# Kernel optimization log

Measured on AMD Instinct MI355X. Metric: run time of the kernel, lower is better.

Reference implementation:

```python
import jax, jax.numpy as jnp
import numpy as np

N, D, B = 100000, 256, 512


def setup_inputs() -> dict:
    key = jax.random.key(0)
    k1, k2, k3, k4, k5 = jax.random.split(key, 5)
    h_fused = jax.random.normal(k1, (N, D), dtype=jnp.float32)
    V = jax.random.normal(k2, (N, D), dtype=jnp.float32)
    bucket_logits_q = jax.random.normal(k3, (N, B), dtype=jnp.float32)
    bk = jax.random.randint(k4, (N,), 0, B, dtype=jnp.int64)
    W_r = jax.random.normal(k5, (D, D), dtype=jnp.float32) * (1.0 / np.sqrt(D))
    ln_gamma = jnp.ones((D,), dtype=jnp.float32)
    ln_beta = jnp.zeros((D,), dtype=jnp.float32)
    return {"h_fused": h_fused, "V": V, "bucket_logits_q": bucket_logits_q,
            "bk": bk, "W_r": W_r, "ln_gamma": ln_gamma, "ln_beta": ln_beta}


def reference(h_fused, V, bucket_logits_q, bk, W_r, ln_gamma, ln_beta):
    n, d = h_fused.shape
    num_buckets = bucket_logits_q.shape[1]

    p_q = jax.nn.softmax(bucket_logits_q, axis=-1)  # (N, B)

    # Single-pass segment-mean replacing the Python per-bucket loop.
    sums = jax.ops.segment_sum(V, bk, num_segments=num_buckets)          # (B, d)
    counts = jax.ops.segment_sum(jnp.ones((n,), V.dtype), bk,
                                 num_segments=num_buckets)               # (B,)
    prototypes = sums / jnp.maximum(counts, 1.0)[:, None]
    global_mean = V.mean(axis=0)
    prototypes = jnp.where((counts == 0)[:, None], global_mean, prototypes)

    proto_weighted = p_q @ prototypes          # (N, d)
    residual = proto_weighted @ W_r.T          # Linear, no bias

    entropy = -(p_q * jnp.log(p_q + 1e-9)).sum(axis=-1)      # (N,)
    confidence = 1.0 - entropy / jnp.log(jnp.float32(num_buckets))
    gate = (1.0 - confidence)[:, None]

    h = h_fused + gate * residual
    # LayerNorm (eps=1e-5, biased variance, as torch)
    mean = h.mean(axis=-1, keepdims=True)
    var = ((h - mean) ** 2).mean(axis=-1, keepdims=True)
    h_norm = (h - mean) / jnp.sqrt(var + 1e-5) * ln_gamma + ln_beta
    return h_norm, confidence
```

## Files before the change

### kernel.cpp

```cpp
#include <hip/hip_runtime.h>
#include <hip/hip_bf16.h>

#define N_ROWS 100000
#define D 256
#define B 512
#define RT 16
#define RS 260

typedef __attribute__((ext_vector_type(8))) short sh8;
typedef __attribute__((ext_vector_type(4))) float f32x4;

__device__ __forceinline__ float lo16(unsigned u) { return __uint_as_float(u << 16); }
__device__ __forceinline__ float hi16(unsigned u) { return __uint_as_float(u & 0xffff0000u); }
__device__ __forceinline__ unsigned short bf16r(float f) {
    unsigned u = __float_as_uint(f);
    unsigned r = (u + 0x7fffu + ((u >> 16) & 1u)) >> 16;
    return (unsigned short)r;
}

template<bool BH>
__device__ __forceinline__ float ldf(const void* p, size_t i) {
    if constexpr (BH) return lo16(((const unsigned short*)p)[i]);
    else              return ((const float*)p)[i];
}
template<bool BH>
__device__ __forceinline__ void ld8(const void* p, size_t i, float* o) {
    if constexpr (BH) {
        uint4 v = *(const uint4*)((const unsigned short*)p + i);
        o[0]=lo16(v.x); o[1]=hi16(v.x); o[2]=lo16(v.y); o[3]=hi16(v.y);
        o[4]=lo16(v.z); o[5]=hi16(v.z); o[6]=lo16(v.w); o[7]=hi16(v.w);
    } else {
        const float4* q = (const float4*)((const float*)p + i);
        float4 a = q[0], b = q[1];
        o[0]=a.x; o[1]=a.y; o[2]=a.z; o[3]=a.w;
        o[4]=b.x; o[5]=b.y; o[6]=b.z; o[7]=b.w;
    }
}
template<bool BH>
__device__ __forceinline__ void stf(void* p, size_t i, float v) {
    if constexpr (BH) ((unsigned short*)p)[i] = bf16r(v);
    else              ((float*)p)[i] = v;
}

__global__ void sniff_kernel(const unsigned* __restrict__ h, int* __restrict__ flag) {
    if (threadIdx.x == 0 && blockIdx.x == 0) {
        int bad = 0;
        for (int i = 0; i < 128; ++i) {
            unsigned w = h[i];
            unsigned e0 = (w >> 7)  & 0xffu;
            unsigned e1 = (w >> 23) & 0xffu;
            if (e0 > 135u || e1 > 135u) bad = 1;
        }
        *flag = bad ? 0 : 1;
    }
}

template<bool BH>
__device__ __forceinline__ void seg_body(const void* __restrict__ V, const void* __restrict__ bkp,
                                         float* __restrict__ sums, float* __restrict__ counts,
                                         float* __restrict__ gsum) {
    bool is64 = true;
    const long long* b64 = (const long long*)bkp;
    #pragma unroll
    for (int j = 0; j < 16; ++j) {
        long long v = b64[j];
        if (v < 0 || v >= B) is64 = false;
    }
    const int* b32 = (const int*)bkp;
    const int t = threadIdx.x;
    float g = 0.f;
    for (int row = blockIdx.x; row < N_ROWS; row += gridDim.x) {
        int k = is64 ? (int)b64[row] : b32[row];
        float v = ldf<BH>(V, (size_t)row * D + t);
        atomicAdd(&sums[k * D + t], v);
        g += v;
        if (t == 0) atomicAdd(&counts[k], 1.0f);
    }
    atomicAdd(&gsum[t], g);
}
__global__ __launch_bounds__(256) void seg_kernel(const void* V, const void* bk,
                                                  float* sums, float* counts, float* gsum,
                                                  const int* flag) {
    if (*flag) seg_body<true>(V, bk, sums, counts, gsum);
    else       seg_body<false>(V, bk, sums, counts, gsum);
}

template<bool BH>
__device__ __forceinline__ void proto_body(const float* __restrict__ sums,
                                           const float* __restrict__ counts,
                                           const float* __restrict__ gsum,
                                           const void* __restrict__ W_r,
                                           unsigned short* __restrict__ pwB,
                                           float* __restrict__ proto) {
    const int b = blockIdx.x, t = threadIdx.x;
    float c = counts[b];
    proto[t] = (c > 0.5f) ? sums[b * D + t] / c : gsum[t] * (1.0f / N_ROWS);
    __syncthreads();
    float acc = 0.f;
    float w[8];
    #pragma unroll
    for (int c8 = 0; c8 < D / 8; ++c8) {
        ld8<BH>(W_r, (size_t)t * D + c8 * 8, w);
        #pragma unroll
        for (int j = 0; j < 8; ++j) acc = fmaf(proto[c8 * 8 + j], w[j], acc);
    }
    pwB[((size_t)(b >> 3) * 256 + t) * 8 + (b & 7)] = bf16r(acc);
}
__global__ __launch_bounds__(256) void proto_kernel(const float* sums, const float* counts,
                                                    const float* gsum, const void* W_r,
                                                    unsigned short* pwB, const int* flag) {
    __shared__ __align__(16) float proto[D];
    if (*flag) proto_body<true>(sums, counts, gsum, W_r, pwB, proto);
    else       proto_body<false>(sums, counts, gsum, W_r, pwB, proto);
}

template<bool BH>
__device__ __forceinline__ void fused_body(const void* __restrict__ logits,
                                           const void* __restrict__ h_fused,
                                           const unsigned short* __restrict__ pwB,
                                           const void* __restrict__ gamma,
                                           const void* __restrict__ beta,
                                           void* __restrict__ out,
                                           float* __restrict__ smu,
                                           float* __restrict__ part1,
                                           float* __restrict__ part2,
                                           float* __restrict__ gate_lds) {
    const int t = threadIdx.x;
    const long long base_row = (long long)blockIdx.x * RT;

    {
        const int grp = t >> 4, sub = t & 15;
        const long long row = base_row + grp;
        float x[32];
        #pragma unroll
        for (int c = 0; c < 4; ++c)
            ld8<BH>(logits, (size_t)row * B + sub * 32 + c * 8, &x[c * 8]);
        float m = x[0];
        #pragma unroll
        for (int k = 1; k < 32; ++k) m = fmaxf(m, x[k]);
        m = fmaxf(m, __shfl_xor(m, 1));
        m = fmaxf(m, __shfl_xor(m, 2));
        m = fmaxf(m, __shfl_xor(m, 4));
        m = fmaxf(m, __shfl_xor(m, 8));
        float S = 0.f;
        #pragma unroll
        for (int k = 0; k < 32; ++k) { x[k] = __expf(x[k] - m); S += x[k]; }
        S += __shfl_xor(S, 1); S += __shfl_xor(S, 2); S += __shfl_xor(S, 4); S += __shfl_xor(S, 8);
        const float inv = 1.0f / S;
        float ent = 0.f;
        #pragma unroll
        for (int k = 0; k < 32; ++k) {
            float p = x[k] * inv;
            ent = fmaf(p, __logf(p + 1e-9f), ent);
            x[k] = p;
        }
        ent += __shfl_xor(ent, 1); ent += __shfl_xor(ent, 2);
        ent += __shfl_xor(ent, 4); ent += __shfl_xor(ent, 8);
        const float gate = -ent * 0.16035674514745464f;
        unsigned short* A16 = (unsigned short*)smu;
        #pragma unroll
        for (int c = 0; c < 4; ++c) {
            unsigned q0 = (unsigned)bf16r(x[c*8+0]) | ((unsigned)bf16r(x[c*8+1]) << 16);
            unsigned q1 = (unsigned)bf16r(x[c*8+2]) | ((unsigned)bf16r(x[c*8+3]) << 16);
            unsigned q2 = (unsigned)bf16r(x[c*8+4]) | ((unsigned)bf16r(x[c*8+5]) << 16);
            unsigned q3 = (unsigned)bf16r(x[c*8+6]) | ((unsigned)bf16r(x[c*8+7]) << 16);
            *(uint4*)&A16[((size_t)(sub * 4 + c) * 16 + grp) * 8] = make_uint4(q0, q1, q2, q3);
        }
        if (sub == 0) {
            gate_lds[grp] = gate;
            stf<BH>(out, (size_t)N_ROWS * D + row, 1.0f - gate);
        }
    }
    __syncthreads();

    {
        const int l  = t & 63, w = t >> 6;
        const int lr = l & 15, lg = l >> 4;
        f32x4 acc[4];
        const f32x4 fz = {0.f, 0.f, 0.f, 0.f};
        #pragma unroll
        for (int n = 0; n < 4; ++n) acc[n] = fz;
        const uint4* Ap = (const uint4*)smu;
        const uint4* Bp = (const uint4*)pwB;
        #pragma unroll 2
        for (int ks = 0; ks < 16; ++ks) {
            const int kg = ks * 4 + lg;
            sh8 a = __builtin_bit_cast(sh8, Ap[kg * 16 + lr]);
            #pragma unroll
            for (int n = 0; n < 4; ++n) {
                sh8 b = __builtin_bit_cast(sh8, Bp[(size_t)kg * 256 + w * 64 + n * 16 + lr]);
                acc[n] = __builtin_amdgcn_mfma_f32_16x16x32_bf16(a, b, acc[n], 0, 0, 0);
            }
        }
        __syncthreads();
        float* res = smu;
        #pragma unroll
        for (int n = 0; n < 4; ++n)
            #pragma unroll
            for (int r = 0; r < 4; ++r)
                res[(lg * 4 + r) * RS + (w * 64 + n * 16 + lr)] = acc[n][r];
    }
    __syncthreads();

    {
        const float* res = smu;
        const float g  = ldf<BH>(gamma, t);
        const float bt = ldf<BH>(beta, t);
        const int wv = t >> 6, ln = t & 63;
        float hr[RT];
        #pragma unroll
        for (int r = 0; r < RT; ++r) {
            const long long row = base_row + r;
            float hv = fmaf(gate_lds[r], res[r * RS + t], ldf<BH>(h_fused, (size_t)row * D + t));
            hr[r] = hv;
            float s1 = hv, s2 = hv * hv;
            #pragma unroll
            for (int o = 32; o > 0; o >>= 1) { s1 += __shfl_xor(s1, o); s2 += __shfl_xor(s2, o); }
            if (ln == 0) { part1[r * 4 + wv] = s1; part2[r * 4 + wv] = s2; }
        }
        __syncthreads();
        #pragma unroll
        for (int r = 0; r < RT; ++r) {
            float sum = part1[r * 4 + 0] + part1[r * 4 + 1] + part1[r * 4 + 2] + part1[r * 4 + 3];
            float sq  = part2[r * 4 + 0] + part2[r * 4 + 1] + part2[r * 4 + 2] + part2[r * 4 + 3];
            float mean = sum * (1.0f / D);
            float var  = fmaf(-mean, mean, sq * (1.0f / D));
            float rstd = rsqrtf(var + 1e-5f);
            const long long row = base_row + r;
            stf<BH>(out, (size_t)row * D + t, fmaf((hr[r] - mean) * rstd, g, bt));
        }
    }
}
__global__ __launch_bounds__(256, 4) void fused_kernel(const void* logits, const void* h_fused,
                                                       const unsigned short* pwB, const void* gamma,
                                                       const void* beta, void* out, const int* flag) {
    __shared__ __align__(16) float sm[RT * RS + RT * 4 * 2 + RT];
    float* smu      = sm;
    float* part1    = sm + RT * RS;
    float* part2    = part1 + RT * 4;
    float* gate_lds = part2 + RT * 4;
    if (*flag) fused_body<true>(logits, h_fused, pwB, gamma, beta, out,
                                smu, part1, part2, gate_lds);
    else       fused_body<false>(logits, h_fused, pwB, gamma, beta, out,
                                 smu, part1, part2, gate_lds);
}

extern "C" void kernel_launch(void* const* d_in, const int* in_sizes, int n_in,
                              void* d_out, int out_size, void* d_ws, size_t ws_size,
                              hipStream_t stream) {
    const void* h_fused = d_in[0];
    const void* V       = d_in[1];
    const void* logits  = d_in[2];
    const void* bk      = d_in[3];
    const void* W_r     = d_in[4];
    const void* gamma   = d_in[5];
    const void* beta    = d_in[6];

    float* ws      = (float*)d_ws;
    float* sums    = ws;
    float* counts  = ws + 131072;
    float* gsum    = ws + 131584;
    unsigned short* pwB = (unsigned short*)(ws + 131840);
    int*   flag    = (int*)(ws + 131840 + 65536);

    hipMemsetAsync(d_ws, 0, (size_t)131840 * sizeof(float), stream);
    sniff_kernel<<<1, 64, 0, stream>>>((const unsigned*)h_fused, flag);
    seg_kernel<<<1024, 256, 0, stream>>>(V, bk, sums, counts, gsum, flag);
    proto_kernel<<<B, 256, 0, stream>>>(sums, counts, gsum, W_r, pwB, flag);
    fused_kernel<<<N_ROWS / RT, 256, 0, stream>>>(logits, h_fused, pwB, gamma, beta, d_out, flag);
}
```

Baseline: 668.9 us.

## Replace atomic segment-sum with counting-sort and per-bucket gather reduction

```diff
diff --git a/kernel.cpp b/kernel.cpp
--- a/kernel.cpp
+++ b/kernel.cpp
@@ -42,6 +42,17 @@
     else              ((float*)p)[i] = v;
 }
 
+__device__ __forceinline__ bool bk_is64(const void* bkp) {
+    bool is64 = true;
+    const long long* b64 = (const long long*)bkp;
+    #pragma unroll
+    for (int j = 0; j < 16; ++j) {
+        long long v = b64[j];
+        if (v < 0 || v >= B) is64 = false;
+    }
+    return is64;
+}
+
 __global__ void sniff_kernel(const unsigned* __restrict__ h, int* __restrict__ flag) {
     if (threadIdx.x == 0 && blockIdx.x == 0) {
         int bad = 0;
@@ -55,34 +66,94 @@
     }
 }
 
-template<bool BH>
-__device__ __forceinline__ void seg_body(const void* __restrict__ V, const void* __restrict__ bkp,
-                                         float* __restrict__ sums, float* __restrict__ counts,
-                                         float* __restrict__ gsum) {
-    bool is64 = true;
+__global__ __launch_bounds__(256) void hist_kernel(const void* __restrict__ bkp,
+                                                   float* __restrict__ counts) {
+    const bool is64 = bk_is64(bkp);
     const long long* b64 = (const long long*)bkp;
+    const int* b32 = (const int*)bkp;
+    const int stride = gridDim.x * 256;
+    for (int row = blockIdx.x * 256 + threadIdx.x; row < N_ROWS; row += stride) {
+        int k = is64 ? (int)b64[row] : b32[row];
+        atomicAdd(&counts[k], 1.0f);
+    }
+}
+
+__global__ __launch_bounds__(512) void scan_kernel(const float* __restrict__ counts,
+                                                   int* __restrict__ offsets,
+                                                   int* __restrict__ cursor) {
+    __shared__ int lds[B];
+    const int t = threadIdx.x;
+    const int c = (int)counts[t];
+    lds[t] = c;
+    __syncthreads();
     #pragma unroll
-    for (int j = 0; j < 16; ++j) {
-        long long v = b64[j];
-        if (v < 0 || v >= B) is64 = false;
-    }
+    for (int off = 1; off < B; off <<= 1) {
+        int v = (t >= off) ? lds[t - off] : 0;
+        __syncthreads();
+        lds[t] += v;
+        __syncthreads();
+    }
+    const int excl = lds[t] - c;
+    offsets[t] = excl;
+    cursor[t]  = excl;
+}
+
+__global__ __launch_bounds__(256) void scatter_kernel(const void* __restrict__ bkp,
+                                                      int* __restrict__ cursor,
+                                                      int* __restrict__ order) {
+    const bool is64 = bk_is64(bkp);
+    const long long* b64 = (const long long*)bkp;
     const int* b32 = (const int*)bkp;
-    const int t = threadIdx.x;
-    float g = 0.f;
-    for (int row = blockIdx.x; row < N_ROWS; row += gridDim.x) {
+    const int stride = gridDim.x * 256;
+    for (int row = blockIdx.x * 256 + threadIdx.x; row < N_ROWS; row += stride) {
         int k = is64 ? (int)b64[row] : b32[row];
-        float v = ldf<BH>(V, (size_t)row * D + t);
-        atomicAdd(&sums[k * D + t], v);
-        g += v;
-        if (t == 0) atomicAdd(&counts[k], 1.0f);
-    }
-    atomicAdd(&gsum[t], g);
-}
-__global__ __launch_bounds__(256) void seg_kernel(const void* V, const void* bk,
-                                                  float* sums, float* counts, float* gsum,
-                                                  const int* flag) {
-    if (*flag) seg_body<true>(V, bk, sums, counts, gsum);
-    else       seg_body<false>(V, bk, sums, counts, gsum);
+        int pos = atomicAdd(&cursor[k], 1);
+        order[pos] = row;
+    }
+}
+
+template<bool BH>
+__device__ __forceinline__ void gather_body(const void* __restrict__ V,
+                                            const int* __restrict__ order,
+                                            const int* __restrict__ offsets,
+                                            const float* __restrict__ counts,
+                                            float* __restrict__ sums,
+                                            float* __restrict__ gsum,
+                                            float* __restrict__ red) {
+    const int b = blockIdx.x;
+    const int start = offsets[b];
+    const int cnt = (int)counts[b];
+    const int col = threadIdx.x & (D - 1);
+    const int half = threadIdx.x >> 8;
+    float acc = 0.f;
+    int i = half;
+    for (; i + 6 < cnt; i += 8) {
+        const int r0 = order[start + i];
+        const int r1 = order[start + i + 2];
+        const int r2 = order[start + i + 4];
+        const int r3 = order[start + i + 6];
+        const float v0 = ldf<BH>(V, (size_t)r0 * D + col);
+        const float v1 = ldf<BH>(V, (size_t)r1 * D + col);
+        const float v2 = ldf<BH>(V, (size_t)r2 * D + col);
+        const float v3 = ldf<BH>(V, (size_t)r3 * D + col);
+        acc += (v0 + v1) + (v2 + v3);
+    }
+    for (; i < cnt; i += 2)
+        acc += ldf<BH>(V, (size_t)order[start + i] * D + col);
+    if (half == 1) red[col] = acc;
+    __syncthreads();
+    if (half == 0) {
+        const float tot = acc + red[col];
+        sums[(size_t)b * D + col] = tot;
+        atomicAdd(&gsum[col], tot);
+    }
+}
+__global__ __launch_bounds__(512) void gather_kernel(const void* V, const int* order,
+                                                     const int* offsets, const float* counts,
+                                                     float* sums, float* gsum, const int* flag) {
+    __shared__ float red[D];
+    if (*flag) gather_body<true>(V, order, offsets, counts, sums, gsum, red);
+    else       gather_body<false>(V, order, offsets, counts, sums, gsum, red);
 }
 
 template<bool BH>
@@ -261,11 +332,17 @@
     float* counts  = ws + 131072;
     float* gsum    = ws + 131584;
     unsigned short* pwB = (unsigned short*)(ws + 131840);
-    int*   flag    = (int*)(ws + 131840 + 65536);
-
-    hipMemsetAsync(d_ws, 0, (size_t)131840 * sizeof(float), stream);
+    int*   order   = (int*)(ws + 131840 + 65536);
+    int*   offsets = order + N_ROWS;
+    int*   cursor  = offsets + B;
+    int*   flag    = cursor + B;
+
+    hipMemsetAsync(counts, 0, (B + D) * sizeof(float), stream);
     sniff_kernel<<<1, 64, 0, stream>>>((const unsigned*)h_fused, flag);
-    seg_kernel<<<1024, 256, 0, stream>>>(V, bk, sums, counts, gsum, flag);
+    hist_kernel<<<256, 256, 0, stream>>>(bk, counts);
+    scan_kernel<<<1, 512, 0, stream>>>(counts, offsets, cursor);
+    scatter_kernel<<<256, 256, 0, stream>>>(bk, cursor, order);
+    gather_kernel<<<B, 512, 0, stream>>>(V, order, offsets, counts, sums, gsum, flag);
     proto_kernel<<<B, 256, 0, stream>>>(sums, counts, gsum, W_r, pwB, flag);
     fused_kernel<<<N_ROWS / RT, 256, 0, stream>>>(logits, h_fused, pwB, gamma, beta, d_out, flag);
 }
```

Result: faster. 630.9 us (-5.7%).
